# Kernel optimization log

Hardware: AMD Instinct MI355X
Metric: run time of the kernel (lower is better)

## Reference

```python
import jax, jax.numpy as jnp
import numpy as np

B, H, KH, D = 32, 32, 8, 128        # requests, q heads, kv heads, head dim
S_CTX = 2049                        # per-request context length (incl. new token)
POOL = B * S_CTX                    # flat token-level KV pool slots


def setup_inputs() -> dict:
    key = jax.random.key(0)
    ks = jax.random.split(key, 5)
    q = jax.random.normal(ks[0], (B, H, D), dtype=jnp.float32)
    k = jax.random.normal(ks[1], (B, KH, D), dtype=jnp.float32)
    v = jax.random.normal(ks[2], (B, KH, D), dtype=jnp.float32)
    k_buffer = jax.random.normal(ks[3], (POOL, KH, D), dtype=jnp.float32)
    v_buffer = jax.random.normal(ks[4], (POOL, KH, D), dtype=jnp.float32)
    # contiguous per-request token layout in the flat pool
    req_to_token = jnp.arange(B * S_CTX, dtype=jnp.int32).reshape(B, S_CTX)
    req_pool_indices = jnp.arange(B, dtype=jnp.int32)
    # new decode token goes into the last slot of each request's row
    out_cache_loc = (jnp.arange(B, dtype=jnp.int32) * S_CTX + (S_CTX - 1)).astype(jnp.int32)
    seq_lens = jnp.full((B,), S_CTX, dtype=jnp.int32)
    return {
        "q": q, "k": k, "v": v,
        "k_buffer": k_buffer, "v_buffer": v_buffer,
        "req_to_token": req_to_token,
        "req_pool_indices": req_pool_indices,
        "out_cache_loc": out_cache_loc,
        "seq_lens": seq_lens,
    }


def reference(q, k, v, k_buffer, v_buffer, req_to_token, req_pool_indices,
              out_cache_loc, seq_lens):
    # set_kv_buffer: write new-token k/v into flat pool at out_cache_loc
    kb = k_buffer.at[out_cache_loc].set(k)
    vb = v_buffer.at[out_cache_loc].set(v)
    # per-request token gather (seq_lens uniform == S_CTX, so full rows)
    tok = req_to_token[req_pool_indices]          # [B, S]
    k_all = kb[tok]                               # [B, S, KH, D]
    v_all = vb[tok]                               # [B, S, KH, D]
    # GQA: q head h attends kv head h // G  (== repeat_interleave on kv heads)
    G = H // KH
    qg = q.reshape(B, KH, G, D)
    scale = 1.0 / jnp.sqrt(jnp.asarray(D, dtype=q.dtype))  # SDPA default scale
    scores = jnp.einsum('bkgd,bskd->bkgs', qg, k_all) * scale  # [B, KH, G, S]
    p = jax.nn.softmax(scores, axis=-1)
    out = jnp.einsum('bkgs,bskd->bkgd', p, v_all)  # [B, KH, G, D]
    return out.reshape(B, H * D)
```

## Files before the change

kernel.cpp:

```cpp
#include <hip/hip_runtime.h>
#include <math.h>

constexpr int KH_ = 8;
constexpr int G_ = 4;
constexpr int D_ = 128;
constexpr int KHD_ = KH_ * D_;
constexpr int HD_ = 32 * 128;
constexpr int WAVES = 16;
constexpr int BLOCK = WAVES * 64;

__global__ void scatter_kv_kernel(const float* __restrict__ k, const float* __restrict__ v,
                                  float* __restrict__ kb, float* __restrict__ vb,
                                  const int* __restrict__ loc, int n) {
    int i = blockIdx.x * blockDim.x + threadIdx.x;
    if (i < n) {
        int b = i / KHD_;
        int off = i - b * KHD_;
        size_t dst = (size_t)loc[b] * KHD_ + off;
        kb[dst] = k[i];
        vb[dst] = v[i];
    }
}

__global__ __launch_bounds__(BLOCK) void attn_decode_kernel(
    const float* __restrict__ q,
    const float* __restrict__ kb,
    const float* __restrict__ vb,
    const int* __restrict__ req_to_token,
    const int* __restrict__ req_pool_indices,
    const int* __restrict__ seq_lens,
    int srt,
    float* __restrict__ out) {
    __shared__ float4 q4[G_ * 32];
    __shared__ float4 p4[WAVES][64];
    __shared__ int    tokl[WAVES][64];
    __shared__ float4 wacc[WAVES][G_][32];
    __shared__ float  wm[WAVES][G_];
    __shared__ float  wl[WAVES][G_];

    const int bid = blockIdx.x;
    const int b = bid / KH_;
    const int kh = bid - b * KH_;
    const int tid = threadIdx.x;
    const int wave = tid >> 6;
    const int lane = tid & 63;

    const int S = seq_lens[b];
    const int rp = req_pool_indices[b];
    const int* __restrict__ tokrow = req_to_token + (size_t)rp * srt;

    const float scale = 0.08838834764831845f;

    if (tid < G_ * 32) {
        const float4* qsrc = (const float4*)(q + (size_t)b * HD_ + (size_t)(kh * G_) * D_);
        float4 t = qsrc[tid];
        t.x *= scale; t.y *= scale; t.z *= scale; t.w *= scale;
        q4[tid] = t;
    }
    __syncthreads();

    float m0 = -INFINITY, m1 = -INFINITY, m2 = -INFINITY, m3 = -INFINITY;
    float l0 = 0.f, l1 = 0.f, l2 = 0.f, l3 = 0.f;
    float4 a0 = {0,0,0,0}, a1 = {0,0,0,0}, a2 = {0,0,0,0}, a3 = {0,0,0,0};

    const int NC = (S + 63) >> 6;
    const int half = lane >> 5;
    const int dq = lane & 31;

    for (int c = wave; c < NC; c += WAVES) {
        const int s = (c << 6) + lane;
        const bool valid = s < S;
        const int tok = tokrow[valid ? s : (S - 1)];
        tokl[wave][lane] = tok;

        const float4* kp = (const float4*)(kb + (size_t)tok * (size_t)KHD_ + (size_t)(kh * D_));
        float s0 = 0.f, s1 = 0.f, s2 = 0.f, s3 = 0.f;
        #pragma unroll 4
        for (int j = 0; j < 32; ++j) {
            const float4 kv = kp[j];
            const float4 qa = q4[j];
            const float4 qb = q4[32 + j];
            const float4 qc = q4[64 + j];
            const float4 qd = q4[96 + j];
            s0 += qa.x*kv.x + qa.y*kv.y + qa.z*kv.z + qa.w*kv.w;
            s1 += qb.x*kv.x + qb.y*kv.y + qb.z*kv.z + qb.w*kv.w;
            s2 += qc.x*kv.x + qc.y*kv.y + qc.z*kv.z + qc.w*kv.w;
            s3 += qd.x*kv.x + qd.y*kv.y + qd.z*kv.z + qd.w*kv.w;
        }
        if (!valid) { s0 = -INFINITY; s1 = -INFINITY; s2 = -INFINITY; s3 = -INFINITY; }

        float c0 = s0, c1 = s1, c2 = s2, c3 = s3;
        #pragma unroll
        for (int off = 32; off > 0; off >>= 1) {
            c0 = fmaxf(c0, __shfl_xor(c0, off));
            c1 = fmaxf(c1, __shfl_xor(c1, off));
            c2 = fmaxf(c2, __shfl_xor(c2, off));
            c3 = fmaxf(c3, __shfl_xor(c3, off));
        }
        const float n0 = fmaxf(m0, c0), n1 = fmaxf(m1, c1), n2 = fmaxf(m2, c2), n3 = fmaxf(m3, c3);
        const float r0 = __expf(m0 - n0), r1 = __expf(m1 - n1), r2 = __expf(m2 - n2), r3 = __expf(m3 - n3);
        m0 = n0; m1 = n1; m2 = n2; m3 = n3;
        float p0 = valid ? __expf(s0 - n0) : 0.f;
        float p1 = valid ? __expf(s1 - n1) : 0.f;
        float p2 = valid ? __expf(s2 - n2) : 0.f;
        float p3 = valid ? __expf(s3 - n3) : 0.f;
        float t0 = p0, t1 = p1, t2s = p2, t3 = p3;
        #pragma unroll
        for (int off = 32; off > 0; off >>= 1) {
            t0 += __shfl_xor(t0, off);
            t1 += __shfl_xor(t1, off);
            t2s += __shfl_xor(t2s, off);
            t3 += __shfl_xor(t3, off);
        }
        l0 = l0 * r0 + t0; l1 = l1 * r1 + t1; l2 = l2 * r2 + t2s; l3 = l3 * r3 + t3;
        p4[wave][lane] = make_float4(p0, p1, p2, p3);

        a0.x *= r0; a0.y *= r0; a0.z *= r0; a0.w *= r0;
        a1.x *= r1; a1.y *= r1; a1.z *= r1; a1.w *= r1;
        a2.x *= r2; a2.y *= r2; a2.z *= r2; a2.w *= r2;
        a3.x *= r3; a3.y *= r3; a3.z *= r3; a3.w *= r3;

        #pragma unroll 4
        for (int t2 = 0; t2 < 32; ++t2) {
            const int idx = (t2 << 1) + half;
            const int tv = tokl[wave][idx];
            const float4 vv = *(const float4*)(vb + (size_t)tv * (size_t)KHD_ + (size_t)(kh * D_) + (dq << 2));
            const float4 pv = p4[wave][idx];
            a0.x += pv.x * vv.x; a0.y += pv.x * vv.y; a0.z += pv.x * vv.z; a0.w += pv.x * vv.w;
            a1.x += pv.y * vv.x; a1.y += pv.y * vv.y; a1.z += pv.y * vv.z; a1.w += pv.y * vv.w;
            a2.x += pv.z * vv.x; a2.y += pv.z * vv.y; a2.z += pv.z * vv.z; a2.w += pv.z * vv.w;
            a3.x += pv.w * vv.x; a3.y += pv.w * vv.y; a3.z += pv.w * vv.z; a3.w += pv.w * vv.w;
        }
    }

    a0.x += __shfl_xor(a0.x, 32); a0.y += __shfl_xor(a0.y, 32); a0.z += __shfl_xor(a0.z, 32); a0.w += __shfl_xor(a0.w, 32);
    a1.x += __shfl_xor(a1.x, 32); a1.y += __shfl_xor(a1.y, 32); a1.z += __shfl_xor(a1.z, 32); a1.w += __shfl_xor(a1.w, 32);
    a2.x += __shfl_xor(a2.x, 32); a2.y += __shfl_xor(a2.y, 32); a2.z += __shfl_xor(a2.z, 32); a2.w += __shfl_xor(a2.w, 32);
    a3.x += __shfl_xor(a3.x, 32); a3.y += __shfl_xor(a3.y, 32); a3.z += __shfl_xor(a3.z, 32); a3.w += __shfl_xor(a3.w, 32);

    if (lane < 32) {
        wacc[wave][0][dq] = a0;
        wacc[wave][1][dq] = a1;
        wacc[wave][2][dq] = a2;
        wacc[wave][3][dq] = a3;
    }
    if (lane == 0) {
        wm[wave][0] = m0; wm[wave][1] = m1; wm[wave][2] = m2; wm[wave][3] = m3;
        wl[wave][0] = l0; wl[wave][1] = l1; wl[wave][2] = l2; wl[wave][3] = l3;
    }
    __syncthreads();

    if (tid < 128) {
        const int g = tid >> 5;
        const int dqq = tid & 31;
        float M = -INFINITY;
        #pragma unroll
        for (int w = 0; w < WAVES; ++w) M = fmaxf(M, wm[w][g]);
        float L = 0.f;
        float4 o = {0,0,0,0};
        #pragma unroll
        for (int w = 0; w < WAVES; ++w) {
            const float f = __expf(wm[w][g] - M);
            L += f * wl[w][g];
            const float4 a = wacc[w][g][dqq];
            o.x += f * a.x; o.y += f * a.y; o.z += f * a.z; o.w += f * a.w;
        }
        const float inv = 1.f / L;
        float4 res;
        res.x = o.x * inv; res.y = o.y * inv; res.z = o.z * inv; res.w = o.w * inv;
        *((float4*)(out + (size_t)b * HD_ + (size_t)(kh * G_ + g) * D_ + (dqq << 2))) = res;
    }
}

extern "C" void kernel_launch(void* const* d_in, const int* in_sizes, int n_in,
                              void* d_out, int out_size, void* d_ws, size_t ws_size,
                              hipStream_t stream) {
    const float* q  = (const float*)d_in[0];
    const float* k  = (const float*)d_in[1];
    const float* v  = (const float*)d_in[2];
    float* kb       = (float*)d_in[3];
    float* vb       = (float*)d_in[4];
    const int* req_to_token     = (const int*)d_in[5];
    const int* req_pool_indices = (const int*)d_in[6];
    const int* out_cache_loc    = (const int*)d_in[7];
    const int* seq_lens         = (const int*)d_in[8];
    float* out = (float*)d_out;

    const int Bn = in_sizes[6];
    const int nscatter = in_sizes[1];
    const int srt = in_sizes[5] / Bn;

    scatter_kv_kernel<<<(nscatter + 255) / 256, 256, 0, stream>>>(k, v, kb, vb, out_cache_loc, nscatter);
    attn_decode_kernel<<<Bn * KH_, BLOCK, 0, stream>>>(q, kb, vb, req_to_token, req_pool_indices,
                                                       seq_lens, srt, out);
}
```

Baseline: 660.0 us.

## Split decode attention across token chunks with a separate combine kernel

Adds a split-K path in which each block processes a chunk of tokens for all KV heads of one request and writes partial max, sum and accumulators to workspace. A second kernel merges the partials with a log-sum-exp rescale. The aim is to fix low occupancy and poor bandwidth use from having only B*KH large blocks. It needs workspace memory and an extra launch, and falls back to the old kernel if the workspace is too small.

```diff
diff --git a/kernel.cpp b/kernel.cpp
--- a/kernel.cpp
+++ b/kernel.cpp
@@ -6,8 +6,7 @@
 constexpr int D_ = 128;
 constexpr int KHD_ = KH_ * D_;
 constexpr int HD_ = 32 * 128;
-constexpr int WAVES = 16;
-constexpr int BLOCK = WAVES * 64;
+constexpr int SLOT_F = 132;
 
 __global__ void scatter_kv_kernel(const float* __restrict__ k, const float* __restrict__ v,
                                   float* __restrict__ kb, float* __restrict__ vb,
@@ -21,6 +20,126 @@
         vb[dst] = v[i];
     }
 }
+
+__global__ __launch_bounds__(256, 6) void attn_partial_kernel(
+    const float* __restrict__ q,
+    const float* __restrict__ kb,
+    const float* __restrict__ vb,
+    const int* __restrict__ req_to_token,
+    const int* __restrict__ req_pool_indices,
+    const int* __restrict__ seq_lens,
+    int srt, int tpb, int nsl,
+    float* __restrict__ ws) {
+    extern __shared__ float sc[];
+
+    const int bid = blockIdx.x;
+    const int b = bid / nsl;
+    const int c = bid - b * nsl;
+    const int T = threadIdx.x;
+    const int kh = T >> 5;
+    const int dq = T & 31;
+
+    const int S = seq_lens[b];
+    const int rp = req_pool_indices[b];
+    const int* __restrict__ tokrow = req_to_token + (size_t)rp * srt;
+    const int t0 = c * tpb;
+    int ntok = S - t0;
+    if (ntok > tpb) ntok = tpb;
+    if (ntok < 0) ntok = 0;
+
+    const float scale = 0.08838834764831845f;
+    const float* qp = q + (size_t)b * HD_ + (size_t)(kh * G_) * D_ + (dq << 2);
+    float4 q0 = *(const float4*)(qp);
+    float4 q1 = *(const float4*)(qp + D_);
+    float4 q2 = *(const float4*)(qp + 2 * D_);
+    float4 q3 = *(const float4*)(qp + 3 * D_);
+    q0.x *= scale; q0.y *= scale; q0.z *= scale; q0.w *= scale;
+    q1.x *= scale; q1.y *= scale; q1.z *= scale; q1.w *= scale;
+    q2.x *= scale; q2.y *= scale; q2.z *= scale; q2.w *= scale;
+    q3.x *= scale; q3.y *= scale; q3.z *= scale; q3.w *= scale;
+
+    #pragma unroll 2
+    for (int t = 0; t < ntok; ++t) {
+        const int tok = tokrow[t0 + t];
+        const float4 kv = *(const float4*)(kb + (size_t)tok * KHD_ + kh * D_ + (dq << 2));
+        float p0 = q0.x * kv.x + q0.y * kv.y + q0.z * kv.z + q0.w * kv.w;
+        float p1 = q1.x * kv.x + q1.y * kv.y + q1.z * kv.z + q1.w * kv.w;
+        float p2 = q2.x * kv.x + q2.y * kv.y + q2.z * kv.z + q2.w * kv.w;
+        float p3 = q3.x * kv.x + q3.y * kv.y + q3.z * kv.z + q3.w * kv.w;
+        #pragma unroll
+        for (int off = 16; off > 0; off >>= 1) {
+            p0 += __shfl_xor(p0, off);
+            p1 += __shfl_xor(p1, off);
+            p2 += __shfl_xor(p2, off);
+            p3 += __shfl_xor(p3, off);
+        }
+        if (dq == 0) *(float4*)&sc[(t << 5) + (kh << 2)] = make_float4(p0, p1, p2, p3);
+    }
+    __syncthreads();
+
+    if (T < 32) {
+        float m = -INFINITY;
+        for (int t = 0; t < ntok; ++t) m = fmaxf(m, sc[(t << 5) + T]);
+        float l = 0.f;
+        for (int t = 0; t < ntok; ++t) {
+            const float p = __expf(sc[(t << 5) + T] - m);
+            l += p;
+            sc[(t << 5) + T] = p;
+        }
+        float* wsl = ws + ((size_t)bid * 32 + T) * SLOT_F;
+        wsl[0] = m;
+        wsl[1] = l;
+    }
+    __syncthreads();
+
+    float4 a0 = {0,0,0,0}, a1 = {0,0,0,0}, a2 = {0,0,0,0}, a3 = {0,0,0,0};
+    #pragma unroll 2
+    for (int t = 0; t < ntok; ++t) {
+        const int tok = tokrow[t0 + t];
+        const float4 vv = *(const float4*)(vb + (size_t)tok * KHD_ + kh * D_ + (dq << 2));
+        const float4 pp = *(const float4*)&sc[(t << 5) + (kh << 2)];
+        a0.x += pp.x * vv.x; a0.y += pp.x * vv.y; a0.z += pp.x * vv.z; a0.w += pp.x * vv.w;
+        a1.x += pp.y * vv.x; a1.y += pp.y * vv.y; a1.z += pp.y * vv.z; a1.w += pp.y * vv.w;
+        a2.x += pp.z * vv.x; a2.y += pp.z * vv.y; a2.z += pp.z * vv.z; a2.w += pp.z * vv.w;
+        a3.x += pp.w * vv.x; a3.y += pp.w * vv.y; a3.z += pp.w * vv.z; a3.w += pp.w * vv.w;
+    }
+
+    float* wsb = ws + (size_t)bid * 32 * SLOT_F + (size_t)(kh << 2) * SLOT_F + 4 + (dq << 2);
+    *(float4*)(wsb)              = a0;
+    *(float4*)(wsb + SLOT_F)     = a1;
+    *(float4*)(wsb + 2 * SLOT_F) = a2;
+    *(float4*)(wsb + 3 * SLOT_F) = a3;
+}
+
+__global__ __launch_bounds__(128) void attn_combine_kernel(
+    const float* __restrict__ ws, float* __restrict__ out, int nsl) {
+    const int bid = blockIdx.x;
+    const int b = bid >> 3;
+    const int kh = bid & 7;
+    const int T = threadIdx.x;
+    const int g = T >> 5;
+    const int dq = T & 31;
+    const size_t slot0 = (size_t)b * nsl * 32 + (kh << 2) + g;
+
+    float M = -INFINITY;
+    for (int c = 0; c < nsl; ++c)
+        M = fmaxf(M, ws[(slot0 + (size_t)c * 32) * SLOT_F]);
+    float L = 0.f;
+    float4 o = {0,0,0,0};
+    for (int c = 0; c < nsl; ++c) {
+        const float* w = ws + (slot0 + (size_t)c * 32) * SLOT_F;
+        const float f = __expf(w[0] - M);
+        L += f * w[1];
+        const float4 a = *(const float4*)(w + 4 + (dq << 2));
+        o.x += f * a.x; o.y += f * a.y; o.z += f * a.z; o.w += f * a.w;
+    }
+    const float inv = 1.f / L;
+    *(float4*)(out + (size_t)b * HD_ + (size_t)((kh << 2) + g) * D_ + (dq << 2)) =
+        make_float4(o.x * inv, o.y * inv, o.z * inv, o.w * inv);
+}
+
+constexpr int WAVES = 16;
+constexpr int BLOCK = WAVES * 64;
 
 __global__ __launch_bounds__(BLOCK) void attn_decode_kernel(
     const float* __restrict__ q,
@@ -48,7 +167,6 @@
     const int S = seq_lens[b];
     const int rp = req_pool_indices[b];
     const int* __restrict__ tokrow = req_to_token + (size_t)rp * srt;
-
     const float scale = 0.08838834764831845f;
 
     if (tid < G_ * 32) {
@@ -62,7 +180,6 @@
     float m0 = -INFINITY, m1 = -INFINITY, m2 = -INFINITY, m3 = -INFINITY;
     float l0 = 0.f, l1 = 0.f, l2 = 0.f, l3 = 0.f;
     float4 a0 = {0,0,0,0}, a1 = {0,0,0,0}, a2 = {0,0,0,0}, a3 = {0,0,0,0};
-
     const int NC = (S + 63) >> 6;
     const int half = lane >> 5;
     const int dq = lane & 31;
@@ -72,7 +189,6 @@
         const bool valid = s < S;
         const int tok = tokrow[valid ? s : (S - 1)];
         tokl[wave][lane] = tok;
-
         const float4* kp = (const float4*)(kb + (size_t)tok * (size_t)KHD_ + (size_t)(kh * D_));
         float s0 = 0.f, s1 = 0.f, s2 = 0.f, s3 = 0.f;
         #pragma unroll 4
@@ -88,7 +204,6 @@
             s3 += qd.x*kv.x + qd.y*kv.y + qd.z*kv.z + qd.w*kv.w;
         }
         if (!valid) { s0 = -INFINITY; s1 = -INFINITY; s2 = -INFINITY; s3 = -INFINITY; }
-
         float c0 = s0, c1 = s1, c2 = s2, c3 = s3;
         #pragma unroll
         for (int off = 32; off > 0; off >>= 1) {
@@ -114,12 +229,10 @@
         }
         l0 = l0 * r0 + t0; l1 = l1 * r1 + t1; l2 = l2 * r2 + t2s; l3 = l3 * r3 + t3;
         p4[wave][lane] = make_float4(p0, p1, p2, p3);
-
         a0.x *= r0; a0.y *= r0; a0.z *= r0; a0.w *= r0;
         a1.x *= r1; a1.y *= r1; a1.z *= r1; a1.w *= r1;
         a2.x *= r2; a2.y *= r2; a2.z *= r2; a2.w *= r2;
         a3.x *= r3; a3.y *= r3; a3.z *= r3; a3.w *= r3;
-
         #pragma unroll 4
         for (int t2 = 0; t2 < 32; ++t2) {
             const int idx = (t2 << 1) + half;
@@ -132,12 +245,10 @@
             a3.x += pv.w * vv.x; a3.y += pv.w * vv.y; a3.z += pv.w * vv.z; a3.w += pv.w * vv.w;
         }
     }
-
     a0.x += __shfl_xor(a0.x, 32); a0.y += __shfl_xor(a0.y, 32); a0.z += __shfl_xor(a0.z, 32); a0.w += __shfl_xor(a0.w, 32);
     a1.x += __shfl_xor(a1.x, 32); a1.y += __shfl_xor(a1.y, 32); a1.z += __shfl_xor(a1.z, 32); a1.w += __shfl_xor(a1.w, 32);
     a2.x += __shfl_xor(a2.x, 32); a2.y += __shfl_xor(a2.y, 32); a2.z += __shfl_xor(a2.z, 32); a2.w += __shfl_xor(a2.w, 32);
     a3.x += __shfl_xor(a3.x, 32); a3.y += __shfl_xor(a3.y, 32); a3.z += __shfl_xor(a3.z, 32); a3.w += __shfl_xor(a3.w, 32);
-
     if (lane < 32) {
         wacc[wave][0][dq] = a0;
         wacc[wave][1][dq] = a1;
@@ -149,7 +260,6 @@
         wl[wave][0] = l0; wl[wave][1] = l1; wl[wave][2] = l2; wl[wave][3] = l3;
     }
     __syncthreads();
-
     if (tid < 128) {
         const int g = tid >> 5;
         const int dqq = tid & 31;
@@ -166,9 +276,8 @@
             o.x += f * a.x; o.y += f * a.y; o.z += f * a.z; o.w += f * a.w;
         }
         const float inv = 1.f / L;
-        float4 res;
-        res.x = o.x * inv; res.y = o.y * inv; res.z = o.z * inv; res.w = o.w * inv;
-        *((float4*)(out + (size_t)b * HD_ + (size_t)(kh * G_ + g) * D_ + (dqq << 2))) = res;
+        *((float4*)(out + (size_t)b * HD_ + (size_t)(kh * G_ + g) * D_ + (dqq << 2))) =
+            make_float4(o.x * inv, o.y * inv, o.z * inv, o.w * inv);
     }
 }
 
@@ -191,6 +300,21 @@
     const int srt = in_sizes[5] / Bn;
 
     scatter_kv_kernel<<<(nscatter + 255) / 256, 256, 0, stream>>>(k, v, kb, vb, out_cache_loc, nscatter);
-    attn_decode_kernel<<<Bn * KH_, BLOCK, 0, stream>>>(q, kb, vb, req_to_token, req_pool_indices,
-                                                       seq_lens, srt, out);
-}
+
+    int tpb = 0, nsl = 0;
+    for (int cand = 32; cand <= 512; cand <<= 1) {
+        const int n = (srt + cand - 1) / cand;
+        const size_t need = (size_t)Bn * n * 32 * (SLOT_F * sizeof(float));
+        if (need <= ws_size) { tpb = cand; nsl = n; break; }
+    }
+
+    if (tpb) {
+        const size_t lds = (size_t)tpb * 32 * sizeof(float);
+        attn_partial_kernel<<<Bn * nsl, 256, lds, stream>>>(
+            q, kb, vb, req_to_token, req_pool_indices, seq_lens, srt, tpb, nsl, (float*)d_ws);
+        attn_combine_kernel<<<Bn * KH_, 128, 0, stream>>>((const float*)d_ws, out, nsl);
+    } else {
+        attn_decode_kernel<<<Bn * KH_, BLOCK, 0, stream>>>(
+            q, kb, vb, req_to_token, req_pool_indices, seq_lens, srt, out);
+    }
+}
```

New measurement: 550.9 us. 1.2x faster.
